# Kernel tuning notes

Hardware: AMD Instinct MI355X
Metric: run time of the kernel (lower is better)

## Reference

```python
import jax, jax.numpy as jnp
import numpy as np

B, L, E = 8, 2048, 4096
TOKEN_DIM, EDGE_DIM, HIDDEN = 768, 256, 128


def setup_inputs() -> dict:
    key = jax.random.key(0)
    k1, k2, k3, k4, k5 = jax.random.split(key, 5)
    token_embedding = jax.random.normal(k1, (B, L, TOKEN_DIM), dtype=jnp.float32)
    edge_embedding = jax.random.normal(k2, (B, E, EDGE_DIM), dtype=jnp.float32)
    # fc: Linear(token_dim+edge_dim -> hidden, bias=False); stored as [in, out]
    W_fc = jax.random.normal(k3, (TOKEN_DIM + EDGE_DIM, HIDDEN), dtype=jnp.float32) * 0.02
    # attn_fc: Linear(2*hidden -> 1); weight flattened to [2*hidden], plus scalar bias
    a_attn = jax.random.normal(k4, (2 * HIDDEN,), dtype=jnp.float32) * 0.02
    b_attn = jax.random.normal(k5, (1,), dtype=jnp.float32) * 0.02
    return {"token_embedding": token_embedding, "edge_embedding": edge_embedding,
            "W_fc": W_fc, "a_attn": a_attn, "b_attn": b_attn}


def reference(token_embedding, edge_embedding, W_fc, a_attn, b_attn):
    # avg edge embedding, broadcast over sequence
    avg_edge = edge_embedding.mean(axis=1, keepdims=True)          # [B, 1, De]
    avg_edge = jnp.broadcast_to(avg_edge, (token_embedding.shape[0],
                                           token_embedding.shape[1],
                                           avg_edge.shape[-1]))     # [B, L, De]
    combined = jnp.concatenate([token_embedding, avg_edge], axis=-1)  # [B, L, Dt+De]
    h = jnp.einsum('bld,dh->blh', combined, W_fc)                   # [B, L, H]

    # Additive attention decomposition: a^T [h_j || h_i] = a1.h_j + a2.h_i
    # (original builds concat([h_repeat_row (=h_j), h_repeat_col (=h_i)]))
    H = h.shape[-1]
    a1, a2 = a_attn[:H], a_attn[H:]
    s_j = jnp.einsum('blh,h->bl', h, a1)                            # score contrib from h_j
    s_i = jnp.einsum('blh,h->bl', h, a2)                            # score contrib from h_i
    scores = s_i[:, :, None] + s_j[:, None, :] + b_attn[0]          # [B, L, L], scores[b,i,j]
    attn = jax.nn.softmax(scores, axis=-1)                          # softmax over j
    h_prime = jnp.einsum('bij,bjh->bih', attn, h)                   # [B, L, H]
    return h_prime
```

## Files before the change

kernel.cpp:

```cpp
#include <hip/hip_runtime.h>

constexpr int Bn  = 8;
constexpr int Ln  = 2048;
constexpr int En  = 4096;
constexpr int TDn = 768;
constexpr int EDn = 256;
constexpr int Hn  = 128;

constexpr int OFF_V1    = 0;
constexpr int OFF_S     = 1024;
constexpr int OFF_EPART = 17408;
constexpr int OFF_TPART = 279552;
constexpr int OFF_T     = 1065984;
constexpr int OFF_ES    = 1072128;
constexpr int OFF_ROW   = 1074176;

__global__ __launch_bounds__(256)
void kA(const float* __restrict__ edge, const float* __restrict__ W,
        const float* __restrict__ a, float* __restrict__ ws) {
    const int tid = threadIdx.x, wv = tid >> 6, q = tid & 63;
    __shared__ float  s_a1[Hn];
    __shared__ float4 s_red[4][64];

    if (blockIdx.x < 3) {
        if (tid < Hn) s_a1[tid] = a[tid];
        __syncthreads();
        int d = blockIdx.x * 256 + tid;
        const float* w = W + d * Hn;
        float acc = 0.f;
        #pragma unroll 8
        for (int h = 0; h < Hn; ++h) acc += w[h] * s_a1[h];
        ws[OFF_V1 + d] = acc;
        return;
    }
    int eb = blockIdx.x - 3;
    int b = eb >> 7, chunk = eb & 127;
    const float4* e4 = (const float4*)edge
                     + ((size_t)(b * En + chunk * 32 + wv * 8)) * (EDn / 4) + q;
    float4 acc = {0.f, 0.f, 0.f, 0.f};
    #pragma unroll
    for (int i = 0; i < 8; ++i) {
        float4 v = e4[(size_t)i * (EDn / 4)];
        acc.x += v.x; acc.y += v.y; acc.z += v.z; acc.w += v.w;
    }
    s_red[wv][q] = acc;
    __syncthreads();
    if (tid < 64) {
        float4 r0 = s_red[0][tid], r1 = s_red[1][tid],
               r2 = s_red[2][tid], r3 = s_red[3][tid];
        float4 s = {r0.x + r1.x + r2.x + r3.x, r0.y + r1.y + r2.y + r3.y,
                    r0.z + r1.z + r2.z + r3.z, r0.w + r1.w + r2.w + r3.w};
        ((float4*)(ws + OFF_EPART))[eb * 64 + tid] = s;
    }
}

__global__ __launch_bounds__(256)
void kB(const float* __restrict__ token, float* __restrict__ ws) {
    __shared__ float4 s_v1[TDn / 4];
    const int tid = threadIdx.x, wv = tid >> 6, lane = tid & 63;
    if (tid < TDn / 4) s_v1[tid] = ((const float4*)(ws + OFF_V1))[tid];
    __syncthreads();
    int row = blockIdx.x * 4 + wv;
    const float4* t4 = (const float4*)token + (size_t)row * (TDn / 4);
    float acc = 0.f;
    #pragma unroll
    for (int j = 0; j < 3; ++j) {
        float4 t = t4[lane + 64 * j];
        float4 v = s_v1[lane + 64 * j];
        acc += t.x * v.x + t.y * v.y + t.z * v.z + t.w * v.w;
    }
    #pragma unroll
    for (int off = 32; off > 0; off >>= 1)
        acc += __shfl_down(acc, off, 64);
    if (lane == 0) ws[OFF_S + row] = acc;
}

__global__ __launch_bounds__(256)
void kC(float* __restrict__ ws) {
    float* s = ws + OFF_S + blockIdx.x * Ln;
    __shared__ float red[256];
    int tid = threadIdx.x;
    float v[8];
    float m = -1e30f;
    #pragma unroll
    for (int k = 0; k < 8; ++k) { v[k] = s[tid + 256 * k]; m = fmaxf(m, v[k]); }
    red[tid] = m; __syncthreads();
    for (int o = 128; o > 0; o >>= 1) {
        if (tid < o) red[tid] = fmaxf(red[tid], red[tid + o]);
        __syncthreads();
    }
    m = red[0]; __syncthreads();
    float sum = 0.f;
    #pragma unroll
    for (int k = 0; k < 8; ++k) { v[k] = expf(v[k] - m); sum += v[k]; }
    red[tid] = sum; __syncthreads();
    for (int o = 128; o > 0; o >>= 1) {
        if (tid < o) red[tid] += red[tid + o];
        __syncthreads();
    }
    float inv = 1.0f / red[0];
    #pragma unroll
    for (int k = 0; k < 8; ++k) s[tid + 256 * k] = v[k] * inv;
}

__global__ __launch_bounds__(192)
void kD(const float* __restrict__ token, float* __restrict__ ws) {
    __shared__ float s_p[16];
    const int tid = threadIdx.x;
    int b = blockIdx.x >> 7, chunk = blockIdx.x & 127;
    if (tid < 16) s_p[tid] = ws[OFF_S + b * Ln + chunk * 16 + tid];
    __syncthreads();
    const float4* t4 = (const float4*)token
                     + ((size_t)(b * Ln + chunk * 16)) * (TDn / 4) + tid;
    float4 acc = {0.f, 0.f, 0.f, 0.f};
    #pragma unroll 4
    for (int l = 0; l < 16; ++l) {
        float4 v = t4[(size_t)l * (TDn / 4)];
        float w = s_p[l];
        acc.x += w * v.x; acc.y += w * v.y; acc.z += w * v.z; acc.w += w * v.w;
    }
    ((float4*)(ws + OFF_TPART))[blockIdx.x * (TDn / 4) + tid] = acc;
}

__global__ __launch_bounds__(256)
void kE1(float* __restrict__ ws) {
    int tid = threadIdx.x;
    if (blockIdx.x < 24) {
        int b = blockIdx.x / 3, part = blockIdx.x % 3;
        int d = part * 256 + tid;
        const float* p = ws + OFF_TPART + (size_t)(b * 128) * TDn + d;
        float acc = 0.f;
        #pragma unroll 4
        for (int ch = 0; ch < 128; ++ch) acc += p[(size_t)ch * TDn];
        ws[OFF_T + b * TDn + d] = acc;
    } else {
        int b = blockIdx.x - 24;
        const float* p = ws + OFF_EPART + (size_t)(b * 128) * EDn + tid;
        float acc = 0.f;
        #pragma unroll 4
        for (int ch = 0; ch < 128; ++ch) acc += p[(size_t)ch * EDn];
        ws[OFF_ES + b * EDn + tid] = acc * (1.0f / En);
    }
}

__global__ __launch_bounds__(1024)
void kE2(const float* __restrict__ W, float* __restrict__ ws) {
    __shared__ float s_c[1024];
    __shared__ float s_red[1024];
    int b = blockIdx.x, tid = threadIdx.x;
    s_c[tid] = (tid < TDn) ? ws[OFF_T + b * TDn + tid]
                           : ws[OFF_ES + b * EDn + (tid - TDn)];
    __syncthreads();
    int h = tid & 127, dg = tid >> 7;
    const float* w = W + (dg * 128) * Hn + h;
    float acc = 0.f;
    #pragma unroll 4
    for (int i = 0; i < 128; ++i)
        acc += s_c[dg * 128 + i] * w[i * Hn];
    s_red[tid] = acc;
    __syncthreads();
    if (tid < 128) {
        float r = 0.f;
        #pragma unroll
        for (int g = 0; g < 8; ++g) r += s_red[g * 128 + tid];
        ws[OFF_ROW + b * Hn + tid] = r;
    }
}

__global__ __launch_bounds__(256)
void kF(const float* __restrict__ ws, float4* __restrict__ out) {
    int idx = blockIdx.x * blockDim.x + threadIdx.x;
    int b = idx >> 16;
    int q = idx & (Hn / 4 - 1);
    out[idx] = ((const float4*)(ws + OFF_ROW))[b * (Hn / 4) + q];
}

extern "C" void kernel_launch(void* const* d_in, const int* in_sizes, int n_in,
                              void* d_out, int out_size, void* d_ws, size_t ws_size,
                              hipStream_t stream) {
    const float* token = (const float*)d_in[0];
    const float* edge  = (const float*)d_in[1];
    const float* W     = (const float*)d_in[2];
    const float* a     = (const float*)d_in[3];
    float* ws  = (float*)d_ws;
    float4* out = (float4*)d_out;

    kA <<<1027,          256, 0, stream>>>(edge, W, a, ws);
    kB <<<Bn * Ln / 4,   256, 0, stream>>>(token, ws);
    kC <<<Bn,            256, 0, stream>>>(ws);
    kD <<<1024,          192, 0, stream>>>(token, ws);
    kE1<<<32,            256, 0, stream>>>(ws);
    kE2<<<Bn,           1024, 0, stream>>>(W, ws);
    kF <<<2048,          256, 0, stream>>>(ws, out);
}
```

Before: 154.0 us.

## Fuse score, softmax and weighted token sum into one chunked online-softmax pass

Score computation, the softmax and the weighted token reduction are merged into one kernel. Each block handles 16 rows, computes a local max and sum, and writes a partial weighted sum of token rows. The final kernel rescales and combines these partials in flash-softmax style, so the token tensor is read once instead of twice and three launches are removed. The v1 projection is also spread over more blocks using wave reductions. The trade-off is a serial 128-chunk rescale loop in a kernel with only 8 blocks.

```diff
diff --git a/kernel.cpp b/kernel.cpp
--- a/kernel.cpp
+++ b/kernel.cpp
@@ -8,42 +8,38 @@
 constexpr int Hn  = 128;
 
 constexpr int OFF_V1    = 0;
-constexpr int OFF_S     = 1024;
-constexpr int OFF_EPART = 17408;
-constexpr int OFF_TPART = 279552;
-constexpr int OFF_T     = 1065984;
-constexpr int OFF_ES    = 1072128;
-constexpr int OFF_ROW   = 1074176;
+constexpr int OFF_EPART = 1024;
+constexpr int OFF_TPART = 263168;
+constexpr int OFF_ROW   = 1053696;
+constexpr int REC = 772;
 
 __global__ __launch_bounds__(256)
-void kA(const float* __restrict__ edge, const float* __restrict__ W,
+void K0(const float* __restrict__ edge, const float* __restrict__ W,
         const float* __restrict__ a, float* __restrict__ ws) {
-    const int tid = threadIdx.x, wv = tid >> 6, q = tid & 63;
-    __shared__ float  s_a1[Hn];
+    const int tid = threadIdx.x, wv = tid >> 6, lane = tid & 63;
     __shared__ float4 s_red[4][64];
 
-    if (blockIdx.x < 3) {
-        if (tid < Hn) s_a1[tid] = a[tid];
-        __syncthreads();
-        int d = blockIdx.x * 256 + tid;
-        const float* w = W + d * Hn;
-        float acc = 0.f;
-        #pragma unroll 8
-        for (int h = 0; h < Hn; ++h) acc += w[h] * s_a1[h];
-        ws[OFF_V1 + d] = acc;
+    if (blockIdx.x < 192) {
+        int d = blockIdx.x * 4 + wv;
+        float acc = W[d * Hn + lane]      * a[lane]
+                  + W[d * Hn + 64 + lane] * a[64 + lane];
+        #pragma unroll
+        for (int off = 32; off > 0; off >>= 1)
+            acc += __shfl_down(acc, off, 64);
+        if (lane == 0) ws[OFF_V1 + d] = acc;
         return;
     }
-    int eb = blockIdx.x - 3;
+    int eb = blockIdx.x - 192;
     int b = eb >> 7, chunk = eb & 127;
     const float4* e4 = (const float4*)edge
-                     + ((size_t)(b * En + chunk * 32 + wv * 8)) * (EDn / 4) + q;
+                     + ((size_t)(b * En + chunk * 32 + wv * 8)) * (EDn / 4) + lane;
     float4 acc = {0.f, 0.f, 0.f, 0.f};
     #pragma unroll
     for (int i = 0; i < 8; ++i) {
         float4 v = e4[(size_t)i * (EDn / 4)];
         acc.x += v.x; acc.y += v.y; acc.z += v.z; acc.w += v.w;
     }
-    s_red[wv][q] = acc;
+    s_red[wv][lane] = acc;
     __syncthreads();
     if (tid < 64) {
         float4 r0 = s_red[0][tid], r1 = s_red[1][tid],
@@ -55,102 +51,96 @@
 }
 
 __global__ __launch_bounds__(256)
-void kB(const float* __restrict__ token, float* __restrict__ ws) {
+void K1(const float* __restrict__ token, float* __restrict__ ws) {
     __shared__ float4 s_v1[TDn / 4];
+    __shared__ float  s_s[16];
+    __shared__ float  s_e[16];
     const int tid = threadIdx.x, wv = tid >> 6, lane = tid & 63;
+    const int b = blockIdx.x >> 7, chunk = blockIdx.x & 127;
+    const size_t row0 = (size_t)(b * Ln + chunk * 16);
+
     if (tid < TDn / 4) s_v1[tid] = ((const float4*)(ws + OFF_V1))[tid];
     __syncthreads();
-    int row = blockIdx.x * 4 + wv;
-    const float4* t4 = (const float4*)token + (size_t)row * (TDn / 4);
-    float acc = 0.f;
+
     #pragma unroll
-    for (int j = 0; j < 3; ++j) {
-        float4 t = t4[lane + 64 * j];
-        float4 v = s_v1[lane + 64 * j];
-        acc += t.x * v.x + t.y * v.y + t.z * v.z + t.w * v.w;
+    for (int i = 0; i < 4; ++i) {
+        int li = wv * 4 + i;
+        const float4* t4 = (const float4*)token + (row0 + li) * (TDn / 4);
+        float acc = 0.f;
+        #pragma unroll
+        for (int j = 0; j < 3; ++j) {
+            float4 t = t4[lane + 64 * j];
+            float4 v = s_v1[lane + 64 * j];
+            acc += t.x * v.x + t.y * v.y + t.z * v.z + t.w * v.w;
+        }
+        #pragma unroll
+        for (int off = 32; off > 0; off >>= 1)
+            acc += __shfl_down(acc, off, 64);
+        if (lane == 0) s_s[li] = acc;
     }
-    #pragma unroll
-    for (int off = 32; off > 0; off >>= 1)
-        acc += __shfl_down(acc, off, 64);
-    if (lane == 0) ws[OFF_S + row] = acc;
-}
+    __syncthreads();
 
-__global__ __launch_bounds__(256)
-void kC(float* __restrict__ ws) {
-    float* s = ws + OFF_S + blockIdx.x * Ln;
-    __shared__ float red[256];
-    int tid = threadIdx.x;
-    float v[8];
     float m = -1e30f;
     #pragma unroll
-    for (int k = 0; k < 8; ++k) { v[k] = s[tid + 256 * k]; m = fmaxf(m, v[k]); }
-    red[tid] = m; __syncthreads();
-    for (int o = 128; o > 0; o >>= 1) {
-        if (tid < o) red[tid] = fmaxf(red[tid], red[tid + o]);
-        __syncthreads();
-    }
-    m = red[0]; __syncthreads();
+    for (int l = 0; l < 16; ++l) m = fmaxf(m, s_s[l]);
+    if (tid < 16) s_e[tid] = expf(s_s[tid] - m);
+    __syncthreads();
+
     float sum = 0.f;
     #pragma unroll
-    for (int k = 0; k < 8; ++k) { v[k] = expf(v[k] - m); sum += v[k]; }
-    red[tid] = sum; __syncthreads();
-    for (int o = 128; o > 0; o >>= 1) {
-        if (tid < o) red[tid] += red[tid + o];
-        __syncthreads();
-    }
-    float inv = 1.0f / red[0];
-    #pragma unroll
-    for (int k = 0; k < 8; ++k) s[tid + 256 * k] = v[k] * inv;
-}
+    for (int l = 0; l < 16; ++l) sum += s_e[l];
 
-__global__ __launch_bounds__(192)
-void kD(const float* __restrict__ token, float* __restrict__ ws) {
-    __shared__ float s_p[16];
-    const int tid = threadIdx.x;
-    int b = blockIdx.x >> 7, chunk = blockIdx.x & 127;
-    if (tid < 16) s_p[tid] = ws[OFF_S + b * Ln + chunk * 16 + tid];
-    __syncthreads();
-    const float4* t4 = (const float4*)token
-                     + ((size_t)(b * Ln + chunk * 16)) * (TDn / 4) + tid;
-    float4 acc = {0.f, 0.f, 0.f, 0.f};
+    const float* tok = token + row0 * TDn;
+    float a0 = 0.f, a1 = 0.f, a2 = 0.f;
     #pragma unroll 4
     for (int l = 0; l < 16; ++l) {
-        float4 v = t4[(size_t)l * (TDn / 4)];
-        float w = s_p[l];
-        acc.x += w * v.x; acc.y += w * v.y; acc.z += w * v.z; acc.w += w * v.w;
+        float e = s_e[l];
+        const float* r = tok + (size_t)l * TDn;
+        a0 += e * r[tid];
+        a1 += e * r[tid + 256];
+        a2 += e * r[tid + 512];
     }
-    ((float4*)(ws + OFF_TPART))[blockIdx.x * (TDn / 4) + tid] = acc;
-}
-
-__global__ __launch_bounds__(256)
-void kE1(float* __restrict__ ws) {
-    int tid = threadIdx.x;
-    if (blockIdx.x < 24) {
-        int b = blockIdx.x / 3, part = blockIdx.x % 3;
-        int d = part * 256 + tid;
-        const float* p = ws + OFF_TPART + (size_t)(b * 128) * TDn + d;
-        float acc = 0.f;
-        #pragma unroll 4
-        for (int ch = 0; ch < 128; ++ch) acc += p[(size_t)ch * TDn];
-        ws[OFF_T + b * TDn + d] = acc;
-    } else {
-        int b = blockIdx.x - 24;
-        const float* p = ws + OFF_EPART + (size_t)(b * 128) * EDn + tid;
-        float acc = 0.f;
-        #pragma unroll 4
-        for (int ch = 0; ch < 128; ++ch) acc += p[(size_t)ch * EDn];
-        ws[OFF_ES + b * EDn + tid] = acc * (1.0f / En);
-    }
+    float* rec = ws + OFF_TPART + (size_t)blockIdx.x * REC;
+    if (tid == 0) { rec[0] = m; rec[1] = sum; }
+    rec[4 + tid]       = a0;
+    rec[4 + tid + 256] = a1;
+    rec[4 + tid + 512] = a2;
 }
 
 __global__ __launch_bounds__(1024)
-void kE2(const float* __restrict__ W, float* __restrict__ ws) {
+void K23(const float* __restrict__ W, float* __restrict__ ws) {
+    __shared__ float s_w[128];
     __shared__ float s_c[1024];
     __shared__ float s_red[1024];
-    int b = blockIdx.x, tid = threadIdx.x;
-    s_c[tid] = (tid < TDn) ? ws[OFF_T + b * TDn + tid]
-                           : ws[OFF_ES + b * EDn + (tid - TDn)];
+    const int b = blockIdx.x, tid = threadIdx.x;
+    const float* recs = ws + OFF_TPART + (size_t)(b * 128) * REC;
+
+    float M = -1e30f;
+    #pragma unroll 4
+    for (int k = 0; k < 128; ++k) M = fmaxf(M, recs[(size_t)k * REC]);
+    float denom = 0.f;
+    #pragma unroll 4
+    for (int k = 0; k < 128; ++k)
+        denom += expf(recs[(size_t)k * REC] - M) * recs[(size_t)k * REC + 1];
+    if (tid < 128) s_w[tid] = expf(recs[(size_t)tid * REC] - M);
     __syncthreads();
+
+    if (tid < TDn) {
+        const float* p = recs + 4 + tid;
+        float acc = 0.f;
+        #pragma unroll 4
+        for (int k = 0; k < 128; ++k) acc += s_w[k] * p[(size_t)k * REC];
+        s_c[tid] = acc / denom;
+    } else {
+        int c = tid - TDn;
+        const float* p = ws + OFF_EPART + (size_t)(b * 128) * EDn + c;
+        float acc = 0.f;
+        #pragma unroll 4
+        for (int k = 0; k < 128; ++k) acc += p[(size_t)k * EDn];
+        s_c[tid] = acc * (1.0f / En);
+    }
+    __syncthreads();
+
     int h = tid & 127, dg = tid >> 7;
     const float* w = W + (dg * 128) * Hn + h;
     float acc = 0.f;
@@ -168,7 +158,7 @@
 }
 
 __global__ __launch_bounds__(256)
-void kF(const float* __restrict__ ws, float4* __restrict__ out) {
+void K4(const float* __restrict__ ws, float4* __restrict__ out) {
     int idx = blockIdx.x * blockDim.x + threadIdx.x;
     int b = idx >> 16;
     int q = idx & (Hn / 4 - 1);
@@ -185,11 +175,8 @@
     float* ws  = (float*)d_ws;
     float4* out = (float4*)d_out;
 
-    kA <<<1027,          256, 0, stream>>>(edge, W, a, ws);
-    kB <<<Bn * Ln / 4,   256, 0, stream>>>(token, ws);
-    kC <<<Bn,            256, 0, stream>>>(ws);
-    kD <<<1024,          192, 0, stream>>>(token, ws);
-    kE1<<<32,            256, 0, stream>>>(ws);
-    kE2<<<Bn,           1024, 0, stream>>>(W, ws);
-    kF <<<2048,          256, 0, stream>>>(ws, out);
+    K0 <<<1216, 256,  0, stream>>>(edge, W, a, ws);
+    K1 <<<1024, 256,  0, stream>>>(token, ws);
+    K23<<<Bn,   1024, 0, stream>>>(W, ws);
+    K4 <<<2048, 256,  0, stream>>>(ws, out);
 }
```

After: 176.1 us. 14.3% more time.
